# Kernel optimization log

Hardware: AMD Instinct MI355X
Metric: run time of the kernel (lower is better)

Reference implementation:

```python
import jax, jax.numpy as jnp
import numpy as np

# Static architecture constants (from init_kwargs)
NUM_AREAS = 4
E_PER = 512          # excitatory units per area
I_PER = 128          # inhibitory units per area
H = NUM_AREAS * (E_PER + I_PER)   # 2560 hidden units
E_SIZE = NUM_AREAS * E_PER        # 2048 = int(0.8 * H)
NUM_OBJS = 2
IN_UNITS = 64
IN_SIZE = NUM_OBJS * IN_UNITS     # 128
ALPHA = 0.02 / 0.1                # dt_x / tau_x


def _build_masks():
    # Recurrent block-connectivity: tridiagonal area graph (adjacent areas connected)
    rec = np.eye(NUM_AREAS) + np.eye(NUM_AREAS, k=1) + np.eye(NUM_AREAS, k=-1)
    ee = np.kron(rec, np.ones((E_PER, E_PER)))
    ie = np.kron(rec, np.ones((I_PER, E_PER)))
    ei = np.kron(np.eye(NUM_AREAS), np.ones((E_PER, I_PER)))
    ii = np.kron(np.eye(NUM_AREAS), np.ones((I_PER, I_PER)))
    conn_rec = np.block([[ee, ei], [ie, ii]])  # rows/cols ordered [all-E | all-I]
    # Dale sign mask: first E_SIZE columns excitatory (+1), rest inhibitory (-1)
    sign = np.concatenate([np.ones(E_SIZE), -np.ones(H - E_SIZE)])[None, :]
    mask_rec = conn_rec * sign
    np.fill_diagonal(mask_rec, 0.0)  # remove_diag=True in h2h EILinear
    # Input connectivity: only area 0 receives external input (e_prop=1 -> all +1)
    in_mask = np.zeros((NUM_AREAS, NUM_OBJS)); in_mask[0, :] = 1.0
    in_e = np.kron(in_mask, np.ones((E_PER, IN_UNITS)))
    in_i = np.kron(in_mask, np.ones((I_PER, IN_UNITS)))
    mask_in = np.vstack([in_e, in_i])
    return jnp.asarray(mask_rec, jnp.float32), jnp.asarray(mask_in, jnp.float32)

MASK_REC, MASK_IN = _build_masks()


def retanh(x):
    return jnp.tanh(jax.nn.relu(x))


def setup_inputs() -> dict:
    key = jax.random.key(0)
    k1, k2, k3 = jax.random.split(key, 3)
    T, B = 32, 64
    x = jax.random.normal(k1, (T, B, IN_SIZE), dtype=jnp.float32)
    # positive-ish inits (original uses gamma; scale ~ 1/sqrt(fan-in))
    W_in = jax.random.uniform(k2, (H, IN_SIZE), dtype=jnp.float32) * 0.02
    W_rec = jax.random.uniform(k3, (H, H), dtype=jnp.float32) * (1.0 / np.sqrt(H))
    b_rec = jnp.zeros((H,), jnp.float32)
    state0 = jnp.zeros((B, H), jnp.float32)
    return {"x": x, "W_in": W_in, "W_rec": W_rec, "b_rec": b_rec, "state0": state0}


def reference(x, W_in, W_rec, b_rec, state0):
    # Effective weights: pos_function='abs' applied to raw weights, then sign/conn mask
    Wr = jnp.abs(W_rec) * MASK_REC          # [H, H]
    Wi = jnp.abs(W_in) * MASK_IN            # [H, IN_SIZE]

    def step(state, xt):
        out = retanh(state)                                # activation of old state
        total = out @ Wr.T + jax.nn.relu(xt) @ Wi.T + b_rec  # h2h(output) + x2h(relu(x)) + bias
        new_state = state * (1.0 - ALPHA) + ALPHA * total    # leaky integration (sigma=0)
        return new_state, retanh(new_state)

    _, outputs = jax.lax.scan(step, state0, x)  # outputs: [T, B, H]
    return outputs
```

## Files before the change

### kernel.cpp

```cpp
#include <hip/hip_runtime.h>
#include <math.h>

#define HH   2560
#define ESZ  2048
#define BB   64
#define TT   32
#define INSZ 128
constexpr float ALPHA_C = 0.2f;

typedef unsigned short ushort_t;
typedef __attribute__((ext_vector_type(8))) unsigned short u16x8;
typedef __attribute__((ext_vector_type(4))) float f32x4;

__device__ __forceinline__ float retanh_f(float v) { return tanhf(fmaxf(v, 0.f)); }
__device__ __forceinline__ ushort_t f2bf(float f) {
    unsigned u = __float_as_uint(f);
    return (ushort_t)((u + 0x7fffu + ((u >> 16) & 1u)) >> 16);
}

__device__ __forceinline__ int area_ne(int a)  { return (a == 1 || a == 2) ? 1536 : 1024; }
__device__ __forceinline__ int area_elo(int a) { return (a > 0 ? a - 1 : 0) << 9; }
__device__ __forceinline__ int area_kc(int a)  { return (a == 0) ? 40 : ((a == 3) ? 36 : 52); }

__global__ __launch_bounds__(256) void wf_pack(const float* __restrict__ Wrec,
                                               const float* __restrict__ Win,
                                               ushort_t* __restrict__ WF) {
    int idx = blockIdx.x * 256 + threadIdx.x;
    int j = idx & 7, l = (idx >> 3) & 63;
    int t = idx >> 9;
    int kc = t % 52, mt = t / 52;
    int area = mt / 40, local = mt - area * 40;
    int ridx = local * 16 + (l & 15);
    int h = (ridx < 512) ? ((area << 9) + ridx) : (ESZ + (area << 7) + (ridx - 512));
    int p = kc * 32 + ((l >> 4) << 3) + j;
    int ne = area_ne(area), elo = area_elo(area);
    int nrec = ne + 128;
    int ntot = nrec + (area == 0 ? 128 : 0);
    float w = 0.f;
    if (p < ne)        { int c = elo + p;                      w = (c == h) ? 0.f :  fabsf(Wrec[(size_t)h * HH + c]); }
    else if (p < nrec) { int c = ESZ + (area << 7) + (p - ne); w = (c == h) ? 0.f : -fabsf(Wrec[(size_t)h * HH + c]); }
    else if (p < ntot) { w = fabsf(Win[(size_t)h * INSZ + (p - nrec)]); }
    WF[idx] = f2bf(w);
}

__global__ __launch_bounds__(256) void xf_pack(const float* __restrict__ x,
                                               ushort_t* __restrict__ xF) {
    int idx = blockIdx.x * 256 + threadIdx.x;
    int j = idx & 7, l = (idx >> 3) & 63;
    int nt = (idx >> 9) & 3, kc = (idx >> 11) & 3, t = idx >> 13;
    int b = nt * 16 + (l & 15);
    int k = kc * 32 + ((l >> 4) << 3) + j;
    xF[idx] = f2bf(fmaxf(x[((size_t)t * BB + b) * INSZ + k], 0.f));
}

__device__ __forceinline__ void act_store(ushort_t* actF, int a, int p, int b, ushort_t v) {
    int kc = p >> 5, kk = p & 31;
    int lane = ((kk >> 3) << 4) + (b & 15);
    actF[(((a * 52 + kc) << 2) + (b >> 4)) * 512 + lane * 8 + (kk & 7)] = v;
}
__device__ __forceinline__ void scatter_act(ushort_t* actF, int h, int b, ushort_t v) {
    if (h < ESZ) {
        int ae = h >> 9;
        int alo = ae > 0 ? ae - 1 : 0, ahi = ae < 3 ? ae + 1 : 3;
        for (int a = alo; a <= ahi; a++) act_store(actF, a, h - area_elo(a), b, v);
    } else {
        int ai = (h - ESZ) >> 7;
        act_store(actF, ai, area_ne(ai) + (h - (ESZ + (ai << 7))), b, v);
    }
}

__global__ __launch_bounds__(256) void init3(const float* __restrict__ state0,
                                             float* __restrict__ stateT,
                                             ushort_t* __restrict__ actF) {
    int idx = blockIdx.x * 256 + threadIdx.x;
    int b = idx / HH, h = idx - b * HH;
    float s = state0[idx];
    int r = (h < ESZ) ? ((h >> 9) * 640 + (h & 511))
                      : (((h - ESZ) >> 7) * 640 + 512 + ((h - ESZ) & 127));
    stateT[r * BB + b] = s;
    scatter_act(actF, h, b, f2bf(retanh_f(s)));
}

__global__ __launch_bounds__(256, 4) void step8(
    const ushort_t* __restrict__ WF,
    const ushort_t* __restrict__ actF_in,
    ushort_t* __restrict__ actF_out,
    const ushort_t* __restrict__ xFt,
    const float* __restrict__ brec,
    float* __restrict__ stateT,
    float* __restrict__ out_t)
{
    __shared__ float part[4 * 256];
    const int tid = threadIdx.x, lane = tid & 63, wv = tid >> 6;
    const int bid = blockIdx.x;
    const int area = (bid >> 1) & 3;
    const int nt   = ((bid >> 2) & 2) | (bid & 1);
    const int ml   = bid >> 4;
    const int mt   = area * 40 + ml;
    const int r0   = area * 640 + ml * 16;
    const int KC   = area_kc(area);
    const int kcx  = (area == 0) ? 36 : 64;

    f32x4 acc = {0.f, 0.f, 0.f, 0.f};
    const ushort_t* aptr = WF + (size_t)mt * 52 * 512 + lane * 8;
    const ushort_t* bbase = actF_in + ((area * 52) * 4 + nt) * 512 + lane * 8;

    for (int kc = wv; kc < KC; kc += 4) {
        u16x8 af = *(const u16x8*)(aptr + (size_t)kc * 512);
        const ushort_t* bp = (kc < kcx) ? (bbase + (size_t)kc * 2048)
                                        : (xFt + ((kc - kcx) * 4 + nt) * 512 + lane * 8);
        u16x8 bf = *(const u16x8*)bp;
        asm volatile("v_mfma_f32_16x16x32_bf16 %0, %1, %2, %0"
                     : "+v"(acc) : "v"(af), "v"(bf));
    }
    asm volatile("s_nop 7\n\ts_nop 7" : "+v"(acc));

#pragma unroll
    for (int i = 0; i < 4; i++)
        part[wv * 256 + (lane & 15) * 16 + ((lane >> 4) << 2) + i] = acc[i];
    __syncthreads();

    {
        const int mm = tid & 15, nn = tid >> 4;
        float s = part[nn * 16 + mm] + part[256 + nn * 16 + mm]
                + part[512 + nn * 16 + mm] + part[768 + nn * 16 + mm];
        const int b = nt * 16 + nn;
        const int ridx = ml * 16 + mm;
        const int h = (ridx < 512) ? ((area << 9) + ridx)
                                   : (ESZ + (area << 7) + (ridx - 512));
        const int r = r0 + mm;
        float st = stateT[r * BB + b];
        float ns = st * (1.f - ALPHA_C) + ALPHA_C * (s + brec[h]);
        stateT[r * BB + b] = ns;
        float o = retanh_f(ns);
        out_t[(size_t)b * HH + h] = o;
        scatter_act(actF_out, h, b, f2bf(o));
    }
}

__device__ __forceinline__ void area_params(int area, int& e_lo, int& n_e,
                                            int& i_lo, int& n_rec, int& n_tot) {
    e_lo = (area > 0 ? area - 1 : 0) << 9;
    int e_hi = ((area < 3 ? area + 1 : 3) + 1) << 9;
    n_e = e_hi - e_lo;
    i_lo = ESZ + (area << 7);
    n_rec = n_e + 128;
    n_tot = n_rec + (area == 0 ? INSZ : 0);
}
__device__ __forceinline__ int row_h(int area, int idx) {
    return (idx < 512) ? ((area << 9) + idx) : (ESZ + (area << 7) + (idx - 512));
}
__global__ __launch_bounds__(256) void init_state2(const float* __restrict__ state0,
                                                   float* __restrict__ stateT,
                                                   float* __restrict__ act0) {
    int idx = blockIdx.x * 256 + threadIdx.x;
    int b = idx / HH, h = idx - b * HH;
    float s = state0[idx];
    int r = (h < ESZ) ? ((h >> 9) * 640 + (h & 511))
                      : (((h - ESZ) >> 7) * 640 + 512 + ((h - ESZ) & 127));
    stateT[r * BB + b] = s;
    act0[((h >> 1) << 7) + b * 2 + (h & 1)] = retanh_f(s);
}
__global__ __launch_bounds__(1024, 4) void step_raw(
    const float* __restrict__ W, const float* __restrict__ Win,
    const float* __restrict__ brec, const float* __restrict__ x_t,
    const float* __restrict__ actIn, float* __restrict__ actOut,
    float* __restrict__ stateT, float* __restrict__ out_t)
{
    __shared__ float part[16 * 680];
    const int tid = threadIdx.x, lane = tid & 63, wv = tid >> 6;
    const int area = blockIdx.x >> 6;
    const int rb = (blockIdx.x & 63) * 10;
    int e_lo, n_e, i_lo, n_rec, n_tot;
    area_params(area, e_lo, n_e, i_lo, n_rec, n_tot);
    const int r0 = area * 640 + rb;
    const int C = n_tot >> 4;
    float2 acc[10];
#pragma unroll
    for (int j = 0; j < 10; j++) acc[j] = make_float2(0.f, 0.f);
    for (int c = wv; c < C; c += 16) {
        const int p0 = c << 4;
        float2 av[8];
        int cbase;
        if (p0 < n_rec) {
            cbase = (p0 < n_e) ? (e_lo + p0) : (i_lo + (p0 - n_e));
            const float* ap = actIn + ((cbase >> 1) << 7) + lane * 2;
#pragma unroll
            for (int i = 0; i < 8; i++) av[i] = *(const float2*)(ap + (i << 7));
        } else {
            cbase = -1;
            const int k0 = p0 - n_rec;
            const float4* xp = (const float4*)(x_t + lane * INSZ + k0);
#pragma unroll
            for (int q = 0; q < 4; q++) {
                float4 v = xp[q];
                av[2 * q]     = make_float2(fmaxf(v.x, 0.f), fmaxf(v.y, 0.f));
                av[2 * q + 1] = make_float2(fmaxf(v.z, 0.f), fmaxf(v.w, 0.f));
            }
        }
#pragma unroll
        for (int j = 0; j < 10; j++) {
            const int h = row_h(area, rb + j);
            const float sgn = (cbase >= 0 && p0 >= n_e) ? -1.f : 1.f;
            const float* wr = (cbase >= 0) ? (W + (size_t)h * HH + cbase)
                                           : (Win + (size_t)h * INSZ + (p0 - n_rec));
#pragma unroll
            for (int i = 0; i < 8; i++) {
                acc[j].x = fmaf(sgn * fabsf(wr[2 * i]),     av[i].x, acc[j].x);
                acc[j].y = fmaf(sgn * fabsf(wr[2 * i + 1]), av[i].y, acc[j].y);
            }
        }
    }
#pragma unroll
    for (int j = 0; j < 10; j++)
        part[wv * 680 + j * 68 + lane] = acc[j].x + acc[j].y;
    __syncthreads();
    int j = -1, b = 0;
    if (tid < 512)      { b = tid >> 3;      j = tid & 7; }
    else if (tid < 640) { int u = tid - 512; b = u >> 1;  j = 8 + (u & 1); }
    if (j >= 0) {
        const int h = row_h(area, rb + j);
        float s = 0.f;
#pragma unroll
        for (int w16 = 0; w16 < 16; w16++) s += part[w16 * 680 + j * 68 + b];
        float sgn = (h < ESZ) ? 1.f : -1.f;
        s -= sgn * fabsf(W[(size_t)h * HH + h]) * actIn[((h >> 1) << 7) + b * 2 + (h & 1)];
        const int r = r0 + j;
        float st = stateT[r * BB + b];
        float ns = st * (1.f - ALPHA_C) + ALPHA_C * (s + brec[h]);
        stateT[r * BB + b] = ns;
        float o = retanh_f(ns);
        out_t[(size_t)b * HH + h] = o;
        actOut[((h >> 1) << 7) + b * 2 + (h & 1)] = o;
    }
}

extern "C" void kernel_launch(void* const* d_in, const int* in_sizes, int n_in,
                              void* d_out, int out_size, void* d_ws, size_t ws_size,
                              hipStream_t stream) {
    const float* x      = (const float*)d_in[0];
    const float* W_in   = (const float*)d_in[1];
    const float* W_rec  = (const float*)d_in[2];
    const float* b_rec  = (const float*)d_in[3];
    const float* state0 = (const float*)d_in[4];
    float* out = (float*)d_out;

    const size_t WFn = (size_t)160 * 52 * 512;
    const size_t xFn = (size_t)TT * 8192;
    const size_t aFn = (size_t)4 * 52 * 4 * 512;
    const size_t need = (WFn + xFn + 2 * aFn) * 2 + (size_t)HH * BB * 4;

    if (ws_size >= need) {
        ushort_t* WF   = (ushort_t*)d_ws;
        ushort_t* xF   = WF + WFn;
        ushort_t* actA = xF + xFn;
        ushort_t* actB = actA + aFn;
        float* stateT  = (float*)(actB + aFn);

        wf_pack<<<16640, 256, 0, stream>>>(W_rec, W_in, WF);
        xf_pack<<<1024, 256, 0, stream>>>(x, xF);
        init3<<<640, 256, 0, stream>>>(state0, stateT, actA);
        for (int t = 0; t < TT; t++) {
            ushort_t* ai = (t & 1) ? actB : actA;
            ushort_t* ao = (t & 1) ? actA : actB;
            step8<<<640, 256, 0, stream>>>(WF, ai, ao, xF + (size_t)t * 8192,
                                           b_rec, stateT, out + (size_t)t * BB * HH);
        }
    } else {
        float* ws = (float*)d_ws;
        const size_t bufElems = (size_t)HH * BB;
        float* stateT = ws;
        float* actA   = stateT + bufElems;
        float* actB   = actA + bufElems;
        init_state2<<<(BB * HH) / 256, 256, 0, stream>>>(state0, stateT, actA);
        for (int t = 0; t < TT; t++) {
            const float* ai = (t & 1) ? actB : actA;
            float* ao       = (t & 1) ? actA : actB;
            step_raw<<<256, 1024, 0, stream>>>(W_rec, W_in, b_rec,
                                               x + (size_t)t * BB * INSZ,
                                               ai, ao, stateT, out + (size_t)t * BB * HH);
        }
    }
}
```

Baseline: 301.3 us.

## Hoist all K-loop loads ahead of MFMAs per area and vectorize weight packing

The step kernel now issues every A/B fragment load for a wave's K-chunks up front into register arrays, with per-area unrolled trip counts, and only then runs the MFMA chain. The previous loop serialized each load with its MFMA. The weight-packing kernel now has each thread produce eight bf16 values and write them as one 16-byte store, which cuts the thread count by eight. The launch-bounds occupancy hint is dropped, which allows higher register use and may lower occupancy.

```diff
diff --git a/kernel.cpp b/kernel.cpp
--- a/kernel.cpp
+++ b/kernel.cpp
@@ -20,27 +20,32 @@
 
 __device__ __forceinline__ int area_ne(int a)  { return (a == 1 || a == 2) ? 1536 : 1024; }
 __device__ __forceinline__ int area_elo(int a) { return (a > 0 ? a - 1 : 0) << 9; }
-__device__ __forceinline__ int area_kc(int a)  { return (a == 0) ? 40 : ((a == 3) ? 36 : 52); }
-
-__global__ __launch_bounds__(256) void wf_pack(const float* __restrict__ Wrec,
-                                               const float* __restrict__ Win,
-                                               ushort_t* __restrict__ WF) {
+
+__global__ __launch_bounds__(256) void wf_pack8(const float* __restrict__ Wrec,
+                                                const float* __restrict__ Win,
+                                                ushort_t* __restrict__ WF) {
     int idx = blockIdx.x * 256 + threadIdx.x;
-    int j = idx & 7, l = (idx >> 3) & 63;
-    int t = idx >> 9;
+    int l = idx & 63;
+    int t = idx >> 6;
     int kc = t % 52, mt = t / 52;
     int area = mt / 40, local = mt - area * 40;
     int ridx = local * 16 + (l & 15);
     int h = (ridx < 512) ? ((area << 9) + ridx) : (ESZ + (area << 7) + (ridx - 512));
-    int p = kc * 32 + ((l >> 4) << 3) + j;
+    int p0 = kc * 32 + ((l >> 4) << 3);
     int ne = area_ne(area), elo = area_elo(area);
     int nrec = ne + 128;
     int ntot = nrec + (area == 0 ? 128 : 0);
-    float w = 0.f;
-    if (p < ne)        { int c = elo + p;                      w = (c == h) ? 0.f :  fabsf(Wrec[(size_t)h * HH + c]); }
-    else if (p < nrec) { int c = ESZ + (area << 7) + (p - ne); w = (c == h) ? 0.f : -fabsf(Wrec[(size_t)h * HH + c]); }
-    else if (p < ntot) { w = fabsf(Win[(size_t)h * INSZ + (p - nrec)]); }
-    WF[idx] = f2bf(w);
+    u16x8 o;
+#pragma unroll
+    for (int j = 0; j < 8; j++) {
+        int p = p0 + j;
+        float w = 0.f;
+        if (p < ne)        { int c = elo + p;                      w = (c == h) ? 0.f :  fabsf(Wrec[(size_t)h * HH + c]); }
+        else if (p < nrec) { int c = ESZ + (area << 7) + (p - ne); w = (c == h) ? 0.f : -fabsf(Wrec[(size_t)h * HH + c]); }
+        else if (p < ntot) { w = fabsf(Win[(size_t)h * INSZ + (p - nrec)]); }
+        o[j] = f2bf(w);
+    }
+    *(u16x8*)(WF + ((size_t)t * 512 + l * 8)) = o;
 }
 
 __global__ __launch_bounds__(256) void xf_pack(const float* __restrict__ x,
@@ -81,7 +86,7 @@
     scatter_act(actF, h, b, f2bf(retanh_f(s)));
 }
 
-__global__ __launch_bounds__(256, 4) void step8(
+__global__ __launch_bounds__(256) void step9(
     const ushort_t* __restrict__ WF,
     const ushort_t* __restrict__ actF_in,
     ushort_t* __restrict__ actF_out,
@@ -98,21 +103,33 @@
     const int ml   = bid >> 4;
     const int mt   = area * 40 + ml;
     const int r0   = area * 640 + ml * 16;
-    const int KC   = area_kc(area);
-    const int kcx  = (area == 0) ? 36 : 64;
 
     f32x4 acc = {0.f, 0.f, 0.f, 0.f};
-    const ushort_t* aptr = WF + (size_t)mt * 52 * 512 + lane * 8;
-    const ushort_t* bbase = actF_in + ((area * 52) * 4 + nt) * 512 + lane * 8;
-
-    for (int kc = wv; kc < KC; kc += 4) {
-        u16x8 af = *(const u16x8*)(aptr + (size_t)kc * 512);
-        const ushort_t* bp = (kc < kcx) ? (bbase + (size_t)kc * 2048)
-                                        : (xFt + ((kc - kcx) * 4 + nt) * 512 + lane * 8);
-        u16x8 bf = *(const u16x8*)bp;
-        asm volatile("v_mfma_f32_16x16x32_bf16 %0, %1, %2, %0"
-                     : "+v"(acc) : "v"(af), "v"(bf));
-    }
+    const ushort_t* aptr = WF + ((size_t)mt * 52 + wv) * 512 + lane * 8;
+    const ushort_t* bptr = actF_in + (((size_t)area * 52 + wv) * 4 + nt) * 512 + lane * 8;
+    const ushort_t* xptr = xFt + ((wv * 4) + nt) * 512 + lane * 8;
+
+#define KLOOP(NIT, HASX)                                                     \
+    {                                                                        \
+        u16x8 af[NIT], bf[NIT];                                              \
+        _Pragma("unroll")                                                    \
+        for (int i = 0; i < (NIT); i++) {                                    \
+            af[i] = *(const u16x8*)(aptr + (size_t)i * 2048);                \
+            bf[i] = ((HASX) && i == (NIT) - 1)                               \
+                        ? *(const u16x8*)xptr                                \
+                        : *(const u16x8*)(bptr + (size_t)i * 8192);          \
+        }                                                                    \
+        _Pragma("unroll")                                                    \
+        for (int i = 0; i < (NIT); i++)                                      \
+            asm volatile("v_mfma_f32_16x16x32_bf16 %0, %1, %2, %0"           \
+                         : "+v"(acc) : "v"(af[i]), "v"(bf[i]));              \
+    }
+
+    if (area == 0)      KLOOP(10, true)
+    else if (area == 3) KLOOP(9,  false)
+    else                KLOOP(13, false)
+#undef KLOOP
+
     asm volatile("s_nop 7\n\ts_nop 7" : "+v"(acc));
 
 #pragma unroll
@@ -257,13 +274,13 @@
         ushort_t* actB = actA + aFn;
         float* stateT  = (float*)(actB + aFn);
 
-        wf_pack<<<16640, 256, 0, stream>>>(W_rec, W_in, WF);
+        wf_pack8<<<2080, 256, 0, stream>>>(W_rec, W_in, WF);
         xf_pack<<<1024, 256, 0, stream>>>(x, xF);
         init3<<<640, 256, 0, stream>>>(state0, stateT, actA);
         for (int t = 0; t < TT; t++) {
             ushort_t* ai = (t & 1) ? actB : actA;
             ushort_t* ao = (t & 1) ? actA : actB;
-            step8<<<640, 256, 0, stream>>>(WF, ai, ao, xF + (size_t)t * 8192,
+            step9<<<640, 256, 0, stream>>>(WF, ai, ao, xF + (size_t)t * 8192,
                                            b_rec, stateT, out + (size_t)t * BB * HH);
         }
     } else {
```

Result: faster. 280.0 us (-7.1%).
